# Kernel tuning notes

Hardware: AMD Instinct MI355X
Metric: run time of the kernel (lower is better)

Reference implementation:

```python
import jax, jax.numpy as jnp
import numpy as np

VOCAB = 185
THRESH = 127.0 / 128.0
S1, S2, S3 = 256, 128, 16
B, L = 262144, 32


def _clamp(x):
    return jnp.clip(x, -THRESH, THRESH)


def setup_inputs() -> dict:
    key = jax.random.key(0)
    ks = jax.random.split(key, 20)
    inp = {
        'pst_idx': jax.random.randint(ks[0], (B, L), 0, 184, dtype=jnp.int64) if jax.config.jax_enable_x64 else jax.random.randint(ks[0], (B, L), 0, 184, dtype=jnp.int32),
        'color_sign': jax.random.normal(ks[1], (B, L), jnp.float32),
        'sob_sign': jax.random.normal(ks[2], (B, L), jnp.float32),
        'wtm': jax.random.uniform(ks[3], (B, 1), jnp.float32),
    }
    isc = 0.72135
    n_symm = 1 + 2 * S1 + 2 * S2
    n_asym = 2 * S1 + S2
    std_s = 1.0 / isc / n_symm ** 0.5
    std_a = 1.0 / isc / n_asym ** 0.5
    std_a2 = 1.0 / isc ** 2 / n_asym ** 0.5
    std_o = 1.0 / isc / (2 * S3) ** 0.5
    std_o2 = 1.0 / isc ** 2 / (2 * S3) ** 0.5
    # embedding tables (divided by 4 as in InputLayer); row 184 is padding (never indexed here)
    inp['emb_fs'] = jax.random.normal(ks[4], (VOCAB, S1), jnp.float32) * 0.25
    inp['emb_va'] = jax.random.normal(ks[5], (VOCAB, S1), jnp.float32) * 0.25
    inp['emb_ha'] = jax.random.normal(ks[6], (VOCAB, S2), jnp.float32) * 0.25
    inp['emb_ra'] = jax.random.normal(ks[7], (VOCAB, S2), jnp.float32) * 0.25
    inp['tempo_w'] = jnp.zeros((S1, 1), jnp.float32)
    # hidden layer weights ([out, in] torch convention)
    inp['fs_w'] = jax.random.normal(ks[8], (S3, S1), jnp.float32) * std_s
    inp['fs_b'] = jax.random.normal(ks[9], (S3,), jnp.float32) * std_s
    inp['absva_w'] = jax.random.normal(ks[10], (S3, S1), jnp.float32) * std_s
    inp['absha_w'] = jax.random.normal(ks[11], (S3, S2), jnp.float32) * std_s
    inp['absra_w'] = jax.random.normal(ks[12], (S3, S2), jnp.float32) * std_s
    inp['va_w'] = jax.random.normal(ks[13], (S3, S1), jnp.float32) * std_a
    inp['fsxva_w'] = jax.random.normal(ks[14], (S3, S1), jnp.float32) * std_a2
    inp['haxra_w'] = jax.random.normal(ks[15], (S3, S2), jnp.float32) * std_a2
    inp['out_va_w'] = jax.random.normal(ks[16], (1, S3), jnp.float32) * std_o
    inp['out_fsxva_w'] = jax.random.normal(ks[17], (1, S3), jnp.float32) * std_o2
    return inp


def _forward(pst_idx, color_sign, sob_sign, wtm, emb_fs, emb_va, emb_ha, emb_ra,
             tempo_w, fs_w, fs_b, absva_w, absha_w, absra_w, va_w, fsxva_w,
             haxra_w, out_va_w, out_fsxva_w):
    b = pst_idx.shape[0]
    rows = jnp.arange(b)[:, None]

    # EmbeddingBag(mode='sum', per_sample_weights=w) == (scatter w into [B,185]) @ table
    def bag(w, table):
        counts = jnp.zeros((b, VOCAB), table.dtype).at[rows, pst_idx].add(w)
        return counts @ table  # [B, s]

    ones = jnp.ones_like(color_sign)
    fs1 = bag(ones, emb_fs)
    va1 = bag(color_sign, emb_va) + wtm @ tempo_w.T
    ha1 = bag(sob_sign, emb_ha)
    ra1 = bag(color_sign * sob_sign, emb_ra)
    fs1, va1, ha1, ra1 = _clamp(fs1), _clamp(va1), _clamp(ha1), _clamp(ra1)

    fs2 = (fs1 @ fs_w.T + fs_b + jnp.abs(va1) @ absva_w.T
           + jnp.abs(ha1) @ absha_w.T + jnp.abs(ra1) @ absra_w.T)
    va2 = va1 @ va_w.T + (fs1 * va1) @ fsxva_w.T + (ha1 * ra1) @ haxra_w.T
    fs2, va2 = _clamp(fs2), _clamp(va2)

    out = va2 @ out_va_w.T + (fs2 * va2) @ out_fsxva_w.T  # [B, 1]
    return jnp.squeeze(out, axis=1)


def reference(pst_idx, color_sign, sob_sign, wtm, emb_fs, emb_va, emb_ha, emb_ra,
              tempo_w, fs_w, fs_b, absva_w, absha_w, absra_w, va_w, fsxva_w,
              haxra_w, out_va_w, out_fsxva_w):
    return _forward(pst_idx, color_sign, sob_sign, wtm, emb_fs, emb_va, emb_ha,
                    emb_ra, tempo_w, fs_w, fs_b, absva_w, absha_w, absra_w,
                    va_w, fsxva_w, haxra_w, out_va_w, out_fsxva_w)
```

## Files before the change

### kernel.cpp

```cpp
#include <hip/hip_runtime.h>
#include <hip/hip_fp16.h>
#include <stdint.h>

typedef _Float16 f16;
typedef _Float16 f16x8 __attribute__((ext_vector_type(8)));
typedef float f32x4 __attribute__((ext_vector_type(4)));

#define NROWS 262144
#define MROWS 16
#define TPB   512
#define GPB   8
#define NBLK  (NROWS / (MROWS * GPB))
#define K     192
#define THR   0.9921875f

#define WS_TABT 0
#define WS_W2FS (768 * 192 * 2)
#define WS_W2VA (WS_W2FS + 16 * 768 * 2)

#define FS_STRIDE 776
#define VA_STRIDE 648
#define VA_BASE   24832
#define EX_BASE   45568
#define PROD_BASE 53760
#define SMEM_SZ   54784

__device__ __forceinline__ f16x8 bc8(uint4 u) {
  union { uint4 u; f16x8 h; } x; x.u = u; return x.h;
}
__device__ __forceinline__ float clampv(float x) {
  return fminf(fmaxf(x, -THR), THR);
}

__global__ void prepack(const float* __restrict__ emb_fs, const float* __restrict__ emb_va,
                        const float* __restrict__ emb_ha, const float* __restrict__ emb_ra,
                        const float* __restrict__ fs_w,   const float* __restrict__ absva_w,
                        const float* __restrict__ absha_w,const float* __restrict__ absra_w,
                        const float* __restrict__ va_w,   const float* __restrict__ fsxva_w,
                        const float* __restrict__ haxra_w, f16* __restrict__ ws) {
  if (blockIdx.x < 24) {
    __shared__ float tile[192 * 33];
    int u0 = blockIdx.x * 32;
    int t = threadIdx.x;
    #pragma unroll 4
    for (int i = 0; i < 24; ++i) {
      int idx = t + 256 * i;
      int k = idx >> 5;
      int c = idx & 31;
      int u = u0 + c;
      float v = 0.f;
      if (k < 185) {
        if      (u < 256) v = emb_fs[k * 256 + u];
        else if (u < 512) v = emb_va[k * 256 + (u - 256)];
        else if (u < 640) v = emb_ha[k * 128 + (u - 512)];
        else              v = emb_ra[k * 128 + (u - 640)];
      }
      tile[k * 33 + c] = v;
    }
    __syncthreads();
    #pragma unroll 4
    for (int i = 0; i < 24; ++i) {
      int idx = t + 256 * i;
      int u = idx / 192;
      int k = idx % 192;
      ws[(u0 + u) * 192 + k] = (f16)tile[k * 33 + u];
    }
  } else {
    int gid = (blockIdx.x - 24) * 256 + threadIdx.x;
    if (gid < 16 * 768) {
      int j = gid / 768, k = gid % 768;
      float v = (k < 256) ? fs_w[j * 256 + k]
              : (k < 512) ? absva_w[j * 256 + (k - 256)]
              : (k < 640) ? absha_w[j * 128 + (k - 512)]
                          : absra_w[j * 128 + (k - 640)];
      ((f16*)((char*)ws + WS_W2FS))[j * 768 + k] = (f16)v;
    } else if (gid < 16 * 768 + 16 * 640) {
      int g = gid - 16 * 768;
      int j = g / 640, k = g % 640;
      float v = (k < 256) ? va_w[j * 256 + k]
              : (k < 512) ? fsxva_w[j * 256 + (k - 256)]
                          : haxra_w[j * 128 + (k - 512)];
      ((f16*)((char*)ws + WS_W2VA))[j * 640 + k] = (f16)v;
    }
  }
}

__global__ __launch_bounds__(TPB, 2)
void rengar_main(const int* __restrict__ pst_idx, const float* __restrict__ color_sign,
                 const float* __restrict__ sob_sign, const float* __restrict__ wtm,
                 const float* __restrict__ tempo_w, const float* __restrict__ fs_b,
                 const float* __restrict__ out_va_w, const float* __restrict__ out_fsxva_w,
                 const f16* __restrict__ ws, float* __restrict__ out) {
  __shared__ __align__(16) char smem[SMEM_SZ];

  const int tid  = threadIdx.x;
  const int lane = tid & 63;
  const int w    = tid >> 6;
  const int l15  = lane & 15;
  const int q    = lane >> 4;

  const f16* tabT = (const f16*)((const char*)ws + WS_TABT);

  uint4 afr1[36];
  int   tbs[6];
  #pragma unroll
  for (int i = 0; i < 6; ++i) {
    int t  = w * 6 + i;
    int u0 = t * 16;
    tbs[i] = (u0 < 256) ? 0 : (u0 < 512) ? 1 : (u0 < 640) ? 2 : 3;
    const f16* ap = tabT + (u0 + l15) * K + q * 8;
    #pragma unroll
    for (int ks = 0; ks < 6; ++ks) afr1[i * 6 + ks] = *(const uint4*)(ap + ks * 32);
  }

  uint4 a2[6];
  if (w < 4) {
    const f16* A = (const f16*)((const char*)ws + WS_W2FS) + l15 * 768 + w * 192 + q * 8;
    #pragma unroll
    for (int ks = 0; ks < 6; ++ks) a2[ks] = *(const uint4*)(A + ks * 32);
  } else {
    const f16* A = (const f16*)((const char*)ws + WS_W2VA) + l15 * 640 + (w - 4) * 160 + q * 8;
    #pragma unroll
    for (int ks = 0; ks < 5; ++ks) a2[ks] = *(const uint4*)(A + ks * 32);
  }

  float bj = 0.f, w1j = 0.f, w2j = 0.f;
  if (tid < 256) {
    int j = tid >> 4;
    bj  = fs_b[j];
    w1j = out_va_w[j];
    w2j = out_fsxva_w[j];
  }

  const int ebase = blockIdx.x * GPB * 512;
  int   vidx = pst_idx[ebase + tid];
  float cc   = color_sign[ebase + tid];
  float ss   = sob_sign[ebase + tid];
  float wtr  = wtm[blockIdx.x * GPB * MROWS + l15];

  #pragma unroll 1
  for (int g = 0; g < GPB; ++g) {
    const int r0 = (blockIdx.x * GPB + g) * MROWS;

    {
      int4 z = make_int4(0, 0, 0, 0);
      int4* p = (int4*)smem;
      #pragma unroll
      for (int i = 0; i < 6; ++i) p[tid + 512 * i] = z;
    }
    __syncthreads();

    {
      int* cntfx = (int*)smem;
      int  row = tid >> 5;
      int* base = cntfx + row * K + vidx;
      atomicAdd(base + 0 * MROWS * K, 65536);
      atomicAdd(base + 1 * MROWS * K, __float2int_rn(cc * 65536.f));
      atomicAdd(base + 2 * MROWS * K, __float2int_rn(ss * 65536.f));
      atomicAdd(base + 3 * MROWS * K, __float2int_rn(cc * ss * 65536.f));
    }
    float nwt = wtr;
    if (g + 1 < GPB) {
      int nb = ebase + (g + 1) * 512;
      vidx = pst_idx[nb + tid];
      cc   = color_sign[nb + tid];
      ss   = sob_sign[nb + tid];
      nwt  = wtm[r0 + MROWS + l15];
    }
    __syncthreads();

    {
      int vals[24];
      const int4* src = (const int4*)smem;
      #pragma unroll
      for (int i = 0; i < 6; ++i) {
        int4 t4 = src[tid * 6 + i];
        vals[4 * i + 0] = t4.x; vals[4 * i + 1] = t4.y;
        vals[4 * i + 2] = t4.z; vals[4 * i + 3] = t4.w;
      }
      __syncthreads();
      int lin = 24 * tid;
      int tb  = lin / 3072;
      int row = (lin / 192) & 15;
      int k0  = lin % 192;
      uint32_t* dst = (uint32_t*)smem + tb * 1600 + row * 100 + (k0 >> 1);
      const float inv = 1.f / 65536.f;
      #pragma unroll
      for (int i = 0; i < 12; ++i) {
        __half2 h = __floats2half2_rn(vals[2 * i] * inv, vals[2 * i + 1] * inv);
        union { __half2 h; uint32_t u; } cv; cv.h = h;
        dst[i] = cv.u;
      }
    }
    __syncthreads();

    f32x4 acc[6];
    {
      uint4 bfr[6];
      int tb_cur = -1;
      #pragma unroll
      for (int i = 0; i < 6; ++i) {
        int tb = tbs[i];
        if (tb != tb_cur) {
          tb_cur = tb;
          #pragma unroll
          for (int ks = 0; ks < 6; ++ks) {
            const uint32_t* p = (const uint32_t*)smem + tb * 1600 + l15 * 100 + ks * 16 + q * 4;
            bfr[ks] = *(const uint4*)p;
          }
        }
        f32x4 a = {0.f, 0.f, 0.f, 0.f};
        #pragma unroll
        for (int ks = 0; ks < 6; ++ks)
          a = __builtin_amdgcn_mfma_f32_16x16x32_f16(bc8(afr1[i * 6 + ks]), bc8(bfr[ks]), a, 0, 0, 0);
        acc[i] = a;
      }
    }
    __syncthreads();

    {
      #pragma unroll
      for (int i = 0; i < 6; ++i) {
        int t  = w * 6 + i;
        int u0 = t * 16;
        int tb = tbs[i];
        int m0 = u0 + q * 4;
        f32x4 a = acc[i];
        if (tb == 0) {
          __half2* d = (__half2*)(smem + l15 * (FS_STRIDE * 2) + m0 * 2);
          d[0] = __floats2half2_rn(clampv(a[0]), clampv(a[1]));
          d[1] = __floats2half2_rn(clampv(a[2]), clampv(a[3]));
        } else if (tb == 1) {
          int s0 = m0 - 256;
          float4 tw = *(const float4*)(tempo_w + s0);
          float b0 = clampv(a[0] + wtr * tw.x);
          float b1 = clampv(a[1] + wtr * tw.y);
          float b2 = clampv(a[2] + wtr * tw.z);
          float b3 = clampv(a[3] + wtr * tw.w);
          __half2* dv = (__half2*)(smem + VA_BASE + l15 * (VA_STRIDE * 2) + s0 * 2);
          dv[0] = __floats2half2_rn(b0, b1);
          dv[1] = __floats2half2_rn(b2, b3);
          __half2* df = (__half2*)(smem + l15 * (FS_STRIDE * 2) + (256 + s0) * 2);
          df[0] = __floats2half2_rn(fabsf(b0), fabsf(b1));
          df[1] = __floats2half2_rn(fabsf(b2), fabsf(b3));
        } else if (tb == 2) {
          int s0 = m0 - 512;
          __half2* d = (__half2*)(smem + l15 * (FS_STRIDE * 2) + (512 + s0) * 2);
          d[0] = __floats2half2_rn(clampv(a[0]), clampv(a[1]));
          d[1] = __floats2half2_rn(clampv(a[2]), clampv(a[3]));
        } else {
          int s0 = m0 - 640;
          __half2* d = (__half2*)(smem + l15 * (FS_STRIDE * 2) + (640 + s0) * 2);
          d[0] = __floats2half2_rn(clampv(a[0]), clampv(a[1]));
          d[1] = __floats2half2_rn(clampv(a[2]), clampv(a[3]));
        }
      }
    }
    __syncthreads();

    {
      uint32_t* fs32 = (uint32_t*)smem;
      uint32_t* va32 = (uint32_t*)(smem + VA_BASE);
      #pragma unroll
      for (int it = 0; it < 6; ++it) {
        int p = tid + 512 * it;
        if (p < 2048) {
          int row = p >> 7, kp = p & 127;
          union { uint32_t u; __half2 h; } a, b, r;
          a.u = fs32[row * 388 + kp];
          b.u = va32[row * 324 + kp];
          r.h = __hmul2(a.h, b.h);
          va32[row * 324 + 128 + kp] = r.u;
        } else {
          int pc = p - 2048;
          int row = pc >> 6, kp = pc & 63;
          union { uint32_t u; __half2 h; } h2, r2, pr;
          h2.u = fs32[row * 388 + 256 + kp];
          r2.u = fs32[row * 388 + 320 + kp];
          pr.h = __hmul2(h2.h, r2.h);
          fs32[row * 388 + 256 + kp] = h2.u & 0x7FFF7FFFu;
          fs32[row * 388 + 320 + kp] = r2.u & 0x7FFF7FFFu;
          va32[row * 324 + 256 + kp] = pr.u;
        }
      }
    }
    __syncthreads();

    float* exch = (float*)(smem + EX_BASE);
    {
      f32x4 a2acc = {0.f, 0.f, 0.f, 0.f};
      if (w < 4) {
        #pragma unroll
        for (int ks = 0; ks < 6; ++ks) {
          int k = w * 192 + ks * 32 + q * 8;
          uint4 bf = *(const uint4*)(smem + l15 * (FS_STRIDE * 2) + k * 2);
          a2acc = __builtin_amdgcn_mfma_f32_16x16x32_f16(bc8(a2[ks]), bc8(bf), a2acc, 0, 0, 0);
        }
      } else {
        #pragma unroll
        for (int ks = 0; ks < 5; ++ks) {
          int k = (w - 4) * 160 + ks * 32 + q * 8;
          uint4 bf = *(const uint4*)(smem + VA_BASE + l15 * (VA_STRIDE * 2) + k * 2);
          a2acc = __builtin_amdgcn_mfma_f32_16x16x32_f16(bc8(a2[ks]), bc8(bf), a2acc, 0, 0, 0);
        }
      }
      #pragma unroll
      for (int r = 0; r < 4; ++r)
        exch[w * 256 + (q * 4 + r) * 16 + l15] = a2acc[r];
    }
    __syncthreads();

    float* prod = (float*)(smem + PROD_BASE);
    if (tid < 256) {
      float f = exch[tid] + exch[256 + tid] + exch[512 + tid] + exch[768 + tid] + bj;
      f = clampv(f);
      float v = exch[1024 + tid] + exch[1280 + tid] + exch[1536 + tid] + exch[1792 + tid];
      v = clampv(v);
      prod[tid] = v * w1j + f * v * w2j;
    }
    __syncthreads();
    if (tid < 16) {
      float s = 0.f;
      #pragma unroll
      for (int j = 0; j < 16; ++j) s += prod[j * 16 + tid];
      out[r0 + tid] = s;
    }
    wtr = nwt;
  }
}

extern "C" void kernel_launch(void* const* d_in, const int* in_sizes, int n_in,
                              void* d_out, int out_size, void* d_ws, size_t ws_size,
                              hipStream_t stream) {
  const int*   pst_idx     = (const int*)  d_in[0];
  const float* color_sign  = (const float*)d_in[1];
  const float* sob_sign    = (const float*)d_in[2];
  const float* wtm         = (const float*)d_in[3];
  const float* emb_fs      = (const float*)d_in[4];
  const float* emb_va      = (const float*)d_in[5];
  const float* emb_ha      = (const float*)d_in[6];
  const float* emb_ra      = (const float*)d_in[7];
  const float* tempo_w     = (const float*)d_in[8];
  const float* fs_b        = (const float*)d_in[10];
  const float* fs_w        = (const float*)d_in[9];
  const float* absva_w     = (const float*)d_in[11];
  const float* absha_w     = (const float*)d_in[12];
  const float* absra_w     = (const float*)d_in[13];
  const float* va_w        = (const float*)d_in[14];
  const float* fsxva_w     = (const float*)d_in[15];
  const float* haxra_w     = (const float*)d_in[16];
  const float* out_va_w    = (const float*)d_in[17];
  const float* out_fsxva_w = (const float*)d_in[18];
  float* out = (float*)d_out;
  f16* ws = (f16*)d_ws;

  prepack<<<24 + 88, 256, 0, stream>>>(emb_fs, emb_va, emb_ha, emb_ra,
                                       fs_w, absva_w, absha_w, absra_w,
                                       va_w, fsxva_w, haxra_w, ws);
  rengar_main<<<NBLK, TPB, 0, stream>>>(pst_idx, color_sign, sob_sign, wtm,
                                        tempo_w, fs_b, out_va_w, out_fsxva_w,
                                        ws, out);
}
```

Measured before the change: 496.2 us.

## Fuse layer-2 reduction via LDS atomics, shuffle output reduce, overlap clearing

Replaces the per-wave exchange buffer and separate product pass with float atomicAdd into swizzled per-row accumulators, then reduces the output with wave shuffles. The count-buffer zeroing moves into the idle upper half of threads during the output phase, and the fp16 repack switches to coalesced strided reads. Together these remove two barriers and shrink shared memory. Launch bounds are raised to 6 blocks per SM, which may force register spills given the large per-thread fragment arrays.

New measurement: 1.711 ms. +244.8%, slower.

```diff
diff --git a/kernel.cpp b/kernel.cpp
--- a/kernel.cpp
+++ b/kernel.cpp
@@ -21,15 +21,17 @@
 #define FS_STRIDE 776
 #define VA_STRIDE 648
 #define VA_BASE   24832
-#define EX_BASE   45568
-#define PROD_BASE 53760
-#define SMEM_SZ   54784
+#define ACC_BASE  49152
+#define SMEM_SZ   51200
 
 __device__ __forceinline__ f16x8 bc8(uint4 u) {
   union { uint4 u; f16x8 h; } x; x.u = u; return x.h;
 }
 __device__ __forceinline__ float clampv(float x) {
   return fminf(fmaxf(x, -THR), THR);
+}
+__device__ __forceinline__ uint32_t packh2(float a, float b) {
+  union { __half2 h; uint32_t u; } cv; cv.h = __floats2half2_rn(a, b); return cv.u;
 }
 
 __global__ void prepack(const float* __restrict__ emb_fs, const float* __restrict__ emb_va,
@@ -85,7 +87,7 @@
   }
 }
 
-__global__ __launch_bounds__(TPB, 2)
+__global__ __launch_bounds__(TPB, 6)
 void rengar_main(const int* __restrict__ pst_idx, const float* __restrict__ color_sign,
                  const float* __restrict__ sob_sign, const float* __restrict__ wtm,
                  const float* __restrict__ tempo_w, const float* __restrict__ fs_b,
@@ -100,6 +102,8 @@
   const int q    = lane >> 4;
 
   const f16* tabT = (const f16*)((const char*)ws + WS_TABT);
+  float* facc = (float*)(smem + ACC_BASE);
+  float* vacc = facc + 256;
 
   uint4 afr1[36];
   int   tbs[6];
@@ -126,7 +130,7 @@
 
   float bj = 0.f, w1j = 0.f, w2j = 0.f;
   if (tid < 256) {
-    int j = tid >> 4;
+    int j = tid & 15;
     bj  = fs_b[j];
     w1j = out_va_w[j];
     w2j = out_fsxva_w[j];
@@ -138,17 +142,20 @@
   float ss   = sob_sign[ebase + tid];
   float wtr  = wtm[blockIdx.x * GPB * MROWS + l15];
 
+  {
+    int4 z = make_int4(0, 0, 0, 0);
+    int4* p = (int4*)smem;
+    #pragma unroll
+    for (int i = 0; i < 7; ++i) {
+      int idx = tid + 512 * i;
+      if (idx < 3200) p[idx] = z;
+    }
+  }
+  __syncthreads();
+
   #pragma unroll 1
   for (int g = 0; g < GPB; ++g) {
     const int r0 = (blockIdx.x * GPB + g) * MROWS;
-
-    {
-      int4 z = make_int4(0, 0, 0, 0);
-      int4* p = (int4*)smem;
-      #pragma unroll
-      for (int i = 0; i < 6; ++i) p[tid + 512 * i] = z;
-    }
-    __syncthreads();
 
     {
       int* cntfx = (int*)smem;
@@ -169,27 +176,28 @@
     }
     __syncthreads();
 
-    {
-      int vals[24];
+    int4 v4[6];
+    {
       const int4* src = (const int4*)smem;
       #pragma unroll
+      for (int i = 0; i < 6; ++i) v4[i] = src[tid + 512 * i];
+    }
+    __syncthreads();
+
+    {
+      const float inv = 1.f / 65536.f;
+      #pragma unroll
       for (int i = 0; i < 6; ++i) {
-        int4 t4 = src[tid * 6 + i];
-        vals[4 * i + 0] = t4.x; vals[4 * i + 1] = t4.y;
-        vals[4 * i + 2] = t4.z; vals[4 * i + 3] = t4.w;
-      }
-      __syncthreads();
-      int lin = 24 * tid;
-      int tb  = lin / 3072;
-      int row = (lin / 192) & 15;
-      int k0  = lin % 192;
-      uint32_t* dst = (uint32_t*)smem + tb * 1600 + row * 100 + (k0 >> 1);
-      const float inv = 1.f / 65536.f;
-      #pragma unroll
-      for (int i = 0; i < 12; ++i) {
-        __half2 h = __floats2half2_rn(vals[2 * i] * inv, vals[2 * i + 1] * inv);
-        union { __half2 h; uint32_t u; } cv; cv.h = h;
-        dst[i] = cv.u;
+        int idx = tid + 512 * i;
+        int tb  = idx / 768;
+        int rem = idx - tb * 768;
+        int row = rem / 48;
+        int k2  = (rem - row * 48) * 2;
+        uint32_t* dst = (uint32_t*)smem + tb * 1600 + row * 100 + k2;
+        uint2 o;
+        o.x = packh2(v4[i].x * inv, v4[i].y * inv);
+        o.y = packh2(v4[i].z * inv, v4[i].w * inv);
+        *(uint2*)dst = o;
       }
     }
     __syncthreads();
@@ -286,7 +294,6 @@
     }
     __syncthreads();
 
-    float* exch = (float*)(smem + EX_BASE);
     {
       f32x4 a2acc = {0.f, 0.f, 0.f, 0.f};
       if (w < 4) {
@@ -304,27 +311,39 @@
           a2acc = __builtin_amdgcn_mfma_f32_16x16x32_f16(bc8(a2[ks]), bc8(bf), a2acc, 0, 0, 0);
         }
       }
-      #pragma unroll
-      for (int r = 0; r < 4; ++r)
-        exch[w * 256 + (q * 4 + r) * 16 + l15] = a2acc[r];
-    }
-    __syncthreads();
-
-    float* prod = (float*)(smem + PROD_BASE);
+      float* dstacc = (w < 4) ? facc : vacc;
+      int base = l15 << 4;
+      #pragma unroll
+      for (int r = 0; r < 4; ++r) {
+        int j = q * 4 + r;
+        atomicAdd(&dstacc[base + ((j + l15) & 15)], a2acc[r]);
+      }
+    }
+    __syncthreads();
+
     if (tid < 256) {
-      float f = exch[tid] + exch[256 + tid] + exch[512 + tid] + exch[768 + tid] + bj;
-      f = clampv(f);
-      float v = exch[1024 + tid] + exch[1280 + tid] + exch[1536 + tid] + exch[1792 + tid];
+      int b = tid >> 4, j = tid & 15;
+      int idx = (b << 4) | ((j + b) & 15);
+      float f = facc[idx];
+      float v = vacc[idx];
+      facc[idx] = 0.f;
+      vacc[idx] = 0.f;
+      f = clampv(f + bj);
       v = clampv(v);
-      prod[tid] = v * w1j + f * v * w2j;
-    }
-    __syncthreads();
-    if (tid < 16) {
-      float s = 0.f;
-      #pragma unroll
-      for (int j = 0; j < 16; ++j) s += prod[j * 16 + tid];
-      out[r0 + tid] = s;
-    }
+      float rr = v * w1j + f * v * w2j;
+      rr += __shfl_xor(rr, 1);
+      rr += __shfl_xor(rr, 2);
+      rr += __shfl_xor(rr, 4);
+      rr += __shfl_xor(rr, 8);
+      if (j == 0) out[r0 + b] = rr;
+    } else if (g + 1 < GPB) {
+      int4 z = make_int4(0, 0, 0, 0);
+      int4* p = (int4*)smem;
+      int t2 = tid - 256;
+      #pragma unroll
+      for (int i = 0; i < 12; ++i) p[t2 + 256 * i] = z;
+    }
+    __syncthreads();
     wtr = nwt;
   }
 }
```
